# Performance work log

Measured on AMD Instinct MI355X. Metric: run time of the kernel, lower is better.

The kernel has to match this reference:

```python
import jax, jax.numpy as jnp
import numpy as np

C, V, T, B = 64, 16000, 64, 8
ALPHA = 1.0  # dt=None -> alpha = 1 (non-trainable buffer)


def setup_inputs() -> dict:
    key = jax.random.key(0)
    k0, k1, k2, k3 = jax.random.split(key, 4)
    tokens = jax.random.randint(k0, (T, B), 0, V)  # time-major [T, B]
    emb_ctx = jax.random.normal(k1, (V, C), dtype=jnp.float32)  # embedding2context
    emb_act = jax.random.normal(k2, (V, C), dtype=jnp.float32)  # embedding2actionable
    bound = 1.0 / np.sqrt(C)
    W_a = jax.random.uniform(k3, (C * V, C), dtype=jnp.float32, minval=-bound, maxval=bound)
    beta_mult = jnp.float32(1.0)
    beta_power = jnp.float32(1.0)
    return {"tokens": tokens, "emb_ctx": emb_ctx, "emb_act": emb_act,
            "W_a": W_a, "beta_mult": beta_mult, "beta_power": beta_power}


def reference(tokens, emb_ctx, emb_act, W_a, beta_mult, beta_power):
    Vv, Cc = emb_ctx.shape
    Tt, Bb = tokens.shape
    # W_a rows are indexed k = v*C + c after .view(-1, V, C)
    W3 = W_a.reshape(Vv, Cc, Cc)  # [V, C, C]

    def step(ctx, tok):
        ce = emb_ctx[tok]  # [B, C] context embedding
        ae = emb_act[tok]  # [B, C] actionable embedding
        ne = jnp.linalg.norm(ce, axis=1, keepdims=True)   # [B, 1]
        nc = jnp.linalg.norm(ctx, axis=1, keepdims=True)  # [B, 1]
        beta = ALPHA * (beta_mult * (ne / (ne + nc))) ** beta_power
        beta = jnp.clip(beta, 0.0, 1.0)
        ctx = (1.0 - beta) * ctx + beta * ce              # norm-gated blend
        # action_map[b,v,c] = sum_d W3[v,c,d] * ctx[b,d]; out[b,v] = sum_c am * ae
        am = jnp.einsum('vcd,bd->bvc', W3, ctx)           # [B, V, C]
        out = jnp.einsum('bvc,bc->bv', am, ae)            # [B, V]
        return ctx, out

    ctx0 = jnp.zeros((Bb, Cc), dtype=emb_ctx.dtype)
    _, outs = jax.lax.scan(step, ctx0, tokens)  # [T, B, V]
    return outs
```

## Files before the change

kernel.cpp:

```cpp
#include <hip/hip_runtime.h>
#include <hip/hip_bf16.h>
#include <stdint.h>

#define T_STEPS 64
#define B_SZ 8
#define C_DIM 64
#define V_SZ 16000
#define K_DIM 4096
#define M_ROWS 512
#define BM 128
#define BN 128
#define BK 32
#define NITER (K_DIM / BK)
#define NWG ((M_ROWS / BM) * (V_SZ / BN))
#define ABYTES 8192
#define WBYTES 16384
#define BUFBYTES (ABYTES + WBYTES)

typedef __bf16 bf16x8 __attribute__((ext_vector_type(8)));
typedef float f32x4 __attribute__((ext_vector_type(4)));

__device__ __forceinline__ void gll16(const void* g, void* l) {
  __builtin_amdgcn_global_load_lds(
      (const __attribute__((address_space(1))) void*)g,
      (__attribute__((address_space(3))) void*)l, 16, 0, 0);
}

__global__ void ctx_kernel(const int* __restrict__ tokens,
                           const float* __restrict__ emb_ctx,
                           const float* __restrict__ beta_mult,
                           const float* __restrict__ beta_power,
                           float* __restrict__ ctx_hist) {
  const int b = blockIdx.x;
  const int d = threadIdx.x;
  const float bm = beta_mult[0];
  const float bp = beta_power[0];
  float ctx = 0.0f;
  for (int t = 0; t < T_STEPS; ++t) {
    const int tok = tokens[t * B_SZ + b];
    const float ce = emb_ctx[tok * C_DIM + d];
    float ne2 = ce * ce;
    float c2 = ctx * ctx;
#pragma unroll
    for (int s = 32; s > 0; s >>= 1) {
      ne2 += __shfl_xor(ne2, s, 64);
      c2 += __shfl_xor(c2, s, 64);
    }
    const float ne = sqrtf(ne2);
    const float nc = sqrtf(c2);
    float beta = powf(bm * (ne / (ne + nc)), bp);
    beta = fminf(fmaxf(beta, 0.0f), 1.0f);
    ctx = (1.0f - beta) * ctx + beta * ce;
    ctx_hist[(t * B_SZ + b) * C_DIM + d] = ctx;
  }
}

__global__ void build_m(const int* __restrict__ tokens,
                        const float* __restrict__ emb_act,
                        const float* __restrict__ ctx_hist,
                        char* __restrict__ Mblk) {
  const int m = blockIdx.x;
  const int tid = threadIdx.x;
  __shared__ float ctxs[C_DIM];
  __shared__ float aes[C_DIM];
  const int t = m >> 3, b = m & 7;
  const int tok = tokens[t * B_SZ + b];
  if (tid < C_DIM) {
    ctxs[tid] = ctx_hist[m * C_DIM + tid];
    aes[tid] = emb_act[tok * C_DIM + tid];
  }
  __syncthreads();
  const int c = tid >> 1;
  const int dh = (tid & 1) * 32;
  const float ae = aes[c];
#pragma unroll
  for (int q = 0; q < 4; ++q) {
    const int k0 = c * C_DIM + dh + q * 8;
    bf16x8 v;
#pragma unroll
    for (int jj = 0; jj < 8; ++jj) v[jj] = (__bf16)(ae * ctxs[dh + q * 8 + jj]);
    *(bf16x8*)(void*)(Mblk + (size_t)(k0 >> 5) * 32768 + ((k0 >> 3) & 3) * 8192 +
                      m * 16) = v;
  }
}

__global__ __launch_bounds__(256, 2)
void gemm_kernel(const char* __restrict__ Ablk, const float* __restrict__ W,
                 float* __restrict__ out) {
  __shared__ __align__(16) char smem[3][BUFBYTES];
  const int tid = threadIdx.x;
  const int lane = tid & 63;
  const int w = tid >> 6;
  const int wm = w >> 1, wn = w & 1;
  const int lrow = lane & 15;
  const int g = lane >> 4;

  const int orig = blockIdx.x;
  const int xcd = orig & 7;
  const int wg = ((xcd < 4) ? xcd * 63 : 252 + (xcd - 4) * 62) + (orig >> 3);
  const int m0 = (wg & 3) * BM;
  const int n0 = (wg >> 2) * BN;

  const char* const abase =
      Ablk + (tid >> 7) * 8192 + (size_t)(m0 + (tid & 127)) * 16;
  const char* const Wc = (const char*)W;
  const int woff = ((tid & 7) * 16) ^ (((tid >> 3) & 7) << 4);
  const char* wbase[4];
#pragma unroll
  for (int s = 0; s < 4; ++s)
    wbase[s] = Wc + (size_t)(n0 + s * 32 + (tid >> 3)) * (K_DIM * 4) + woff;

  auto STAGE = [&](int b, int kt) {
    char* dst = smem[b];
#pragma unroll
    for (int s = 0; s < 2; ++s)
      gll16(abase + (size_t)kt * 32768 + s * 16384, dst + s * 4096 + tid * 16);
#pragma unroll
    for (int s = 0; s < 4; ++s)
      gll16(wbase[s] + (size_t)kt * 128, dst + ABYTES + s * 4096 + tid * 16);
  };

  f32x4 acc[4][4];
#pragma unroll
  for (int fm = 0; fm < 4; ++fm)
#pragma unroll
    for (int fn = 0; fn < 4; ++fn) acc[fm][fn] = (f32x4){0.f, 0.f, 0.f, 0.f};

  auto COMPUTE = [&](int b) {
    const char* Ab = smem[b];
    const char* Wb = smem[b] + ABYTES;
    bf16x8 a[4];
#pragma unroll
    for (int fm = 0; fm < 4; ++fm)
      a[fm] = *(const bf16x8*)(Ab + g * 2048 + (wm * 64 + fm * 16 + lrow) * 16);
#pragma unroll
    for (int fn = 0; fn < 4; ++fn) {
      const int col = wn * 64 + fn * 16 + lrow;
      const int xo = (col & 7) << 4;
      const f32x4 b0 = *(const f32x4*)(Wb + col * 128 + ((g * 32) ^ xo));
      const f32x4 b1 = *(const f32x4*)(Wb + col * 128 + ((g * 32 + 16) ^ xo));
      bf16x8 bv;
#pragma unroll
      for (int j = 0; j < 4; ++j) {
        bv[j] = (__bf16)b0[j];
        bv[4 + j] = (__bf16)b1[j];
      }
#pragma unroll
      for (int fm = 0; fm < 4; ++fm)
        acc[fm][fn] =
            __builtin_amdgcn_mfma_f32_16x16x32_bf16(a[fm], bv, acc[fm][fn], 0, 0, 0);
    }
  };

  STAGE(0, 0);
  STAGE(1, 1);

  int cur = 0;
#pragma unroll 1
  for (int kt = 0; kt < NITER - 2; ++kt) {
    const int stg = (cur == 0) ? 2 : cur - 1;
    STAGE(stg, kt + 2);
    asm volatile("s_waitcnt vmcnt(12)" ::: "memory");
    __builtin_amdgcn_s_barrier();
    COMPUTE(cur);
    __builtin_amdgcn_s_barrier();
    cur = (cur == 2) ? 0 : cur + 1;
  }
  asm volatile("s_waitcnt vmcnt(6)" ::: "memory");
  __builtin_amdgcn_s_barrier();
  COMPUTE(cur);
  __builtin_amdgcn_s_barrier();
  cur = (cur == 2) ? 0 : cur + 1;
  asm volatile("s_waitcnt vmcnt(0)" ::: "memory");
  __builtin_amdgcn_s_barrier();
  COMPUTE(cur);

#pragma unroll
  for (int fm = 0; fm < 4; ++fm)
#pragma unroll
    for (int q = 0; q < 4; ++q) {
      const int row = m0 + wm * 64 + fm * 16 + g * 4 + q;
      float* po = out + (size_t)row * V_SZ + n0 + wn * 64 + lrow;
#pragma unroll
      for (int fn = 0; fn < 4; ++fn) po[fn * 16] = acc[fm][fn][q];
    }
}

extern "C" void kernel_launch(void* const* d_in, const int* in_sizes, int n_in,
                              void* d_out, int out_size, void* d_ws, size_t ws_size,
                              hipStream_t stream) {
  const int* tokens = (const int*)d_in[0];
  const float* emb_ctx = (const float*)d_in[1];
  const float* emb_act = (const float*)d_in[2];
  const float* W = (const float*)d_in[3];
  const float* beta_mult = (const float*)d_in[4];
  const float* beta_power = (const float*)d_in[5];
  float* out = (float*)d_out;

  char* Mblk = (char*)d_ws;
  float* ctx_hist = (float*)((char*)d_ws + (size_t)M_ROWS * K_DIM * 2);

  ctx_kernel<<<B_SZ, C_DIM, 0, stream>>>(tokens, emb_ctx, beta_mult, beta_power,
                                         ctx_hist);
  build_m<<<M_ROWS, 128, 0, stream>>>(tokens, emb_act, ctx_hist, Mblk);
  gemm_kernel<<<NWG, 256, 0, stream>>>(Mblk, W, out);
}
```

Before: 193.6 us.

## Shrink GEMM N-tile to 64, double-buffer, swizzle A in LDS

Halves the GEMM tile width to 64 columns, moves from triple to double buffering, and raises the occupancy hint to 4 workgroups per CU. It also adds an XOR swizzle to the A tile layout in LDS to cut bank conflicts, and simplifies the XCD-aware workgroup remap. The goal is more waves in flight and more workgroups to hide memory latency. In exchange, each workgroup reuses less data per tile, so the A operand is re-read twice as often, and the prefetch depth is shallower.

```diff
diff --git a/kernel.cpp b/kernel.cpp
--- a/kernel.cpp
+++ b/kernel.cpp
@@ -9,12 +9,12 @@
 #define K_DIM 4096
 #define M_ROWS 512
 #define BM 128
-#define BN 128
+#define BN 64
 #define BK 32
 #define NITER (K_DIM / BK)
 #define NWG ((M_ROWS / BM) * (V_SZ / BN))
 #define ABYTES 8192
-#define WBYTES 16384
+#define WBYTES 8192
 #define BUFBYTES (ABYTES + WBYTES)
 
 typedef __bf16 bf16x8 __attribute__((ext_vector_type(8)));
@@ -84,10 +84,10 @@
   }
 }
 
-__global__ __launch_bounds__(256, 2)
+__global__ __launch_bounds__(256, 4)
 void gemm_kernel(const char* __restrict__ Ablk, const float* __restrict__ W,
                  float* __restrict__ out) {
-  __shared__ __align__(16) char smem[3][BUFBYTES];
+  __shared__ __align__(16) char smem[2][BUFBYTES];
   const int tid = threadIdx.x;
   const int lane = tid & 63;
   const int w = tid >> 6;
@@ -95,47 +95,52 @@
   const int lrow = lane & 15;
   const int g = lane >> 4;
 
-  const int orig = blockIdx.x;
-  const int xcd = orig & 7;
-  const int wg = ((xcd < 4) ? xcd * 63 : 252 + (xcd - 4) * 62) + (orig >> 3);
+  const int wg = (blockIdx.x & 7) * (NWG / 8) + (blockIdx.x >> 3);
   const int m0 = (wg & 3) * BM;
   const int n0 = (wg >> 2) * BN;
 
-  const char* const abase =
-      Ablk + (tid >> 7) * 8192 + (size_t)(m0 + (tid & 127)) * 16;
-  const char* const Wc = (const char*)W;
-  const int woff = ((tid & 7) * 16) ^ (((tid >> 3) & 7) << 4);
-  const char* wbase[4];
-#pragma unroll
-  for (int s = 0; s < 4; ++s)
-    wbase[s] = Wc + (size_t)(n0 + s * 32 + (tid >> 3)) * (K_DIM * 4) + woff;
+  const char* asrc[2];
+#pragma unroll
+  for (int s = 0; s < 2; ++s) {
+    const int L = s * 4096 + tid * 16;
+    const int ga = L >> 11;
+    const int row = ((L & 2047) ^ (ga << 5)) >> 4;
+    asrc[s] = Ablk + ga * 8192 + (size_t)(m0 + row) * 16;
+  }
+  const char* wsrc[2];
+#pragma unroll
+  for (int s = 0; s < 2; ++s) {
+    const int col = s * 32 + (tid >> 3);
+    const int koff = ((tid & 7) * 16) ^ ((col & 7) << 4);
+    wsrc[s] = (const char*)W + (size_t)(n0 + col) * (K_DIM * 4) + koff;
+  }
 
   auto STAGE = [&](int b, int kt) {
     char* dst = smem[b];
-#pragma unroll
-    for (int s = 0; s < 2; ++s)
-      gll16(abase + (size_t)kt * 32768 + s * 16384, dst + s * 4096 + tid * 16);
-#pragma unroll
-    for (int s = 0; s < 4; ++s)
-      gll16(wbase[s] + (size_t)kt * 128, dst + ABYTES + s * 4096 + tid * 16);
+    gll16(asrc[0] + (size_t)kt * 32768, dst + tid * 16);
+    gll16(asrc[1] + (size_t)kt * 32768, dst + 4096 + tid * 16);
+    gll16(wsrc[0] + (size_t)kt * 128, dst + ABYTES + tid * 16);
+    gll16(wsrc[1] + (size_t)kt * 128, dst + ABYTES + 4096 + tid * 16);
   };
 
-  f32x4 acc[4][4];
+  f32x4 acc[4][2];
 #pragma unroll
   for (int fm = 0; fm < 4; ++fm)
 #pragma unroll
-    for (int fn = 0; fn < 4; ++fn) acc[fm][fn] = (f32x4){0.f, 0.f, 0.f, 0.f};
+    for (int fn = 0; fn < 2; ++fn) acc[fm][fn] = (f32x4){0.f, 0.f, 0.f, 0.f};
 
   auto COMPUTE = [&](int b) {
     const char* Ab = smem[b];
     const char* Wb = smem[b] + ABYTES;
     bf16x8 a[4];
 #pragma unroll
-    for (int fm = 0; fm < 4; ++fm)
-      a[fm] = *(const bf16x8*)(Ab + g * 2048 + (wm * 64 + fm * 16 + lrow) * 16);
-#pragma unroll
-    for (int fn = 0; fn < 4; ++fn) {
-      const int col = wn * 64 + fn * 16 + lrow;
+    for (int fm = 0; fm < 4; ++fm) {
+      const int row = wm * 64 + fm * 16 + lrow;
+      a[fm] = *(const bf16x8*)(Ab + g * 2048 + ((row * 16) ^ (g << 5)));
+    }
+#pragma unroll
+    for (int fn = 0; fn < 2; ++fn) {
+      const int col = wn * 32 + fn * 16 + lrow;
       const int xo = (col & 7) << 4;
       const f32x4 b0 = *(const f32x4*)(Wb + col * 128 + ((g * 32) ^ xo));
       const f32x4 b1 = *(const f32x4*)(Wb + col * 128 + ((g * 32 + 16) ^ xo));
@@ -153,24 +158,16 @@
   };
 
   STAGE(0, 0);
-  STAGE(1, 1);
-
   int cur = 0;
 #pragma unroll 1
-  for (int kt = 0; kt < NITER - 2; ++kt) {
-    const int stg = (cur == 0) ? 2 : cur - 1;
-    STAGE(stg, kt + 2);
-    asm volatile("s_waitcnt vmcnt(12)" ::: "memory");
+  for (int kt = 0; kt < NITER - 1; ++kt) {
+    STAGE(cur ^ 1, kt + 1);
+    asm volatile("s_waitcnt vmcnt(4)" ::: "memory");
     __builtin_amdgcn_s_barrier();
     COMPUTE(cur);
     __builtin_amdgcn_s_barrier();
-    cur = (cur == 2) ? 0 : cur + 1;
-  }
-  asm volatile("s_waitcnt vmcnt(6)" ::: "memory");
-  __builtin_amdgcn_s_barrier();
-  COMPUTE(cur);
-  __builtin_amdgcn_s_barrier();
-  cur = (cur == 2) ? 0 : cur + 1;
+    cur ^= 1;
+  }
   asm volatile("s_waitcnt vmcnt(0)" ::: "memory");
   __builtin_amdgcn_s_barrier();
   COMPUTE(cur);
@@ -180,9 +177,9 @@
 #pragma unroll
     for (int q = 0; q < 4; ++q) {
       const int row = m0 + wm * 64 + fm * 16 + g * 4 + q;
-      float* po = out + (size_t)row * V_SZ + n0 + wn * 64 + lrow;
-#pragma unroll
-      for (int fn = 0; fn < 4; ++fn) po[fn * 16] = acc[fm][fn][q];
+      float* po = out + (size_t)row * V_SZ + n0 + wn * 32 + lrow;
+      po[0] = acc[fm][0][q];
+      po[16] = acc[fm][1][q];
     }
 }
 
```

Result: slower. 219.8 us (+13.5%).
